# Optimization experiments

Measured on AMD Instinct MI355X. Metric: run time of the kernel, lower is better.

The kernel has to match this reference:

```python
import jax, jax.numpy as jnp
import numpy as np

K = 3  # spatial window (window_size = [1,3,3,1])


def _extract_patches(x, k):
    """TF-style extract_patches, VALID padding, stride 1, rate 1.
    x: [B,H,W,C] -> [B,Ho,Wo,k*k*C] with depth ordering (ki, kj, c)."""
    B, H, W, C = x.shape
    Ho, Wo = H - k + 1, W - k + 1
    cols = [x[:, ki:ki + Ho, kj:kj + Wo, :] for ki in range(k) for kj in range(k)]
    return jnp.concatenate(cols, axis=-1)


def setup_inputs() -> dict:
    key = jax.random.key(0)
    k1, k2 = jax.random.split(key)
    x = jax.random.normal(k1, (8, 32, 32, 32), dtype=jnp.float32)
    # weight shape per build(): (1, 1, 1, K*K*C, filters) = (1,1,1,288,64)
    w = jax.random.normal(k2, (1, 1, 1, 3 * 3 * 32, 64), dtype=jnp.float32) * 0.05
    bias = jnp.zeros((64,), dtype=jnp.float32)
    return {"x": x, "w": w, "bias": bias}


def reference(x, w, bias):
    # patches: [B,Ho,Wo,KKC]
    p = _extract_patches(x, K)
    # broadcast add: [B,Ho,Wo,KKC,1] + [KKC,F] -> [B,Ho,Wo,KKC,F]
    r = p[..., None] + w[0, 0, 0]
    # tropical conv: max-plus minus min-plus over the patch axis, plus bias
    return jnp.max(r, axis=3) - jnp.min(r, axis=3) + bias
```

## Files before the change

### kernel.cpp

```cpp
#include <hip/hip_runtime.h>
#include <math.h>


__global__ __launch_bounds__(256) void trop_kernel(
    const float* __restrict__ x, const float* __restrict__ w,
    const float* __restrict__ bias, float* __restrict__ out) {
  __shared__ float wl[96 * 64];

  const int jg = blockIdx.x;
  const int i = blockIdx.y;
  const int b = blockIdx.z;
  const int tid = threadIdx.x;
  const int f = tid & 63;
  const int jwu = __builtin_amdgcn_readfirstlane(tid >> 6) * 4;
  const int j0 = jg * 14 + jwu;

  float mx[4] = {-INFINITY, -INFINITY, -INFINITY, -INFINITY};
  float mn[4] = {INFINITY, INFINITY, INFINITY, INFINITY};

  for (int ki = 0; ki < 3; ++ki) {
    __syncthreads();
    const float4* wg = (const float4*)(w + ki * 96 * 64);
    float4* wld = (float4*)wl;
#pragma unroll
    for (int t = 0; t < 6; ++t) wld[tid + t * 256] = wg[tid + t * 256];
    __syncthreads();

    const float* xr = x + (((size_t)b * 32 + (i + ki)) * 32 + j0) * 32;

#pragma unroll
    for (int c8 = 0; c8 < 32; c8 += 8) {
      float4 xa[6][2];
#pragma unroll
      for (int col = 0; col < 6; ++col) {
        xa[col][0] = *(const float4*)(xr + col * 32 + c8);
        xa[col][1] = *(const float4*)(xr + col * 32 + c8 + 4);
      }
      const float* wbase = &wl[c8 * 64 + f];
#pragma unroll
      for (int c = 0; c < 8; ++c) {
        float w0 = wbase[c * 64];
        float w1 = wbase[32 * 64 + c * 64];
        float w2 = wbase[64 * 64 + c * 64];
        float xv[6];
#pragma unroll
        for (int col = 0; col < 6; ++col)
          xv[col] = ((const float*)xa[col])[c];
#pragma unroll
        for (int p = 0; p < 4; ++p) {
          float a0 = xv[p + 0] + w0;
          float a1 = xv[p + 1] + w1;
          float a2 = xv[p + 2] + w2;
          mx[p] = fmaxf(mx[p], fmaxf(a0, fmaxf(a1, a2)));
          mn[p] = fminf(mn[p], fminf(a0, fminf(a1, a2)));
        }
      }
    }
  }

  float bv = bias[f];
  float* ob = out + (((size_t)b * 30 + i) * 30 + j0) * 64 + f;
#pragma unroll
  for (int p = 0; p < 4; ++p) ob[p * 64] = mx[p] - mn[p] + bv;
}

extern "C" void kernel_launch(void* const* d_in, const int* in_sizes, int n_in,
                              void* d_out, int out_size, void* d_ws, size_t ws_size,
                              hipStream_t stream) {
  const float* x = (const float*)d_in[0];
  const float* w = (const float*)d_in[1];
  const float* bias = (const float*)d_in[2];
  float* out = (float*)d_out;
  dim3 grid(2, 30, 8);
  dim3 block(256);
  hipLaunchKernelGGL(trop_kernel, grid, block, 0, stream, x, w, bias, out);
}
```

Baseline: 69.60 us.

## Transpose weights in LDS per filter and cover full row per 512-thread block

Stores the weight slice in LDS transposed per filter with a padded stride so each thread reads its weights as float4 vectors instead of scalar strided loads. Each block now has 8 waves covering a whole output row (32 columns, with clamping and masked stores for the 30 valid ones), halving the grid and the number of times weights are staged into LDS. The transposed layout costs uncoalesced scalar global weight loads during staging and some wasted work on the padded columns.

```diff
diff --git a/kernel.cpp b/kernel.cpp
--- a/kernel.cpp
+++ b/kernel.cpp
@@ -2,55 +2,69 @@
 #include <math.h>
 
 
-__global__ __launch_bounds__(256) void trop_kernel(
+#define WSTRIDE 100
+
+__global__ __launch_bounds__(512) void trop_kernel(
     const float* __restrict__ x, const float* __restrict__ w,
     const float* __restrict__ bias, float* __restrict__ out) {
-  __shared__ float wl[96 * 64];
+  __shared__ float wt[64 * WSTRIDE];
 
-  const int jg = blockIdx.x;
-  const int i = blockIdx.y;
-  const int b = blockIdx.z;
+  const int i = blockIdx.x;
+  const int b = blockIdx.y;
   const int tid = threadIdx.x;
   const int f = tid & 63;
-  const int jwu = __builtin_amdgcn_readfirstlane(tid >> 6) * 4;
-  const int j0 = jg * 14 + jwu;
+  const int j0 = __builtin_amdgcn_readfirstlane(tid >> 6) * 4;
+
+  const int skq = tid >> 6;
 
   float mx[4] = {-INFINITY, -INFINITY, -INFINITY, -INFINITY};
   float mn[4] = {INFINITY, INFINITY, INFINITY, INFINITY};
+  float bv = bias[f];
 
   for (int ki = 0; ki < 3; ++ki) {
     __syncthreads();
-    const float4* wg = (const float4*)(w + ki * 96 * 64);
-    float4* wld = (float4*)wl;
 #pragma unroll
-    for (int t = 0; t < 6; ++t) wld[tid + t * 256] = wg[tid + t * 256];
+    for (int it = 0; it < 3; ++it) {
+      int k0 = (it * 8 + skq) * 4;
+      float4 v;
+      v.x = w[(ki * 96 + k0 + 0) * 64 + f];
+      v.y = w[(ki * 96 + k0 + 1) * 64 + f];
+      v.z = w[(ki * 96 + k0 + 2) * 64 + f];
+      v.w = w[(ki * 96 + k0 + 3) * 64 + f];
+      *(float4*)(&wt[f * WSTRIDE + k0]) = v;
+    }
     __syncthreads();
 
-    const float* xr = x + (((size_t)b * 32 + (i + ki)) * 32 + j0) * 32;
+    const float* xr = x + (((size_t)b * 32 + (i + ki)) * 32) * 32;
+    int cc[6];
+#pragma unroll
+    for (int col = 0; col < 6; ++col) cc[col] = (j0 + col < 32) ? j0 + col : 31;
 
 #pragma unroll
     for (int c8 = 0; c8 < 32; c8 += 8) {
       float4 xa[6][2];
 #pragma unroll
       for (int col = 0; col < 6; ++col) {
-        xa[col][0] = *(const float4*)(xr + col * 32 + c8);
-        xa[col][1] = *(const float4*)(xr + col * 32 + c8 + 4);
+        xa[col][0] = *(const float4*)(xr + cc[col] * 32 + c8);
+        xa[col][1] = *(const float4*)(xr + cc[col] * 32 + c8 + 4);
       }
-      const float* wbase = &wl[c8 * 64 + f];
+      float4 wv[3][2];
+#pragma unroll
+      for (int kj = 0; kj < 3; ++kj) {
+        const float* wrow = &wt[f * WSTRIDE + kj * 32 + c8];
+        wv[kj][0] = *(const float4*)(wrow);
+        wv[kj][1] = *(const float4*)(wrow + 4);
+      }
 #pragma unroll
       for (int c = 0; c < 8; ++c) {
-        float w0 = wbase[c * 64];
-        float w1 = wbase[32 * 64 + c * 64];
-        float w2 = wbase[64 * 64 + c * 64];
-        float xv[6];
-#pragma unroll
-        for (int col = 0; col < 6; ++col)
-          xv[col] = ((const float*)xa[col])[c];
+        float w0 = ((const float*)&wv[0][0])[c];
+        float w1 = ((const float*)&wv[1][0])[c];
+        float w2 = ((const float*)&wv[2][0])[c];
 #pragma unroll
         for (int p = 0; p < 4; ++p) {
-          float a0 = xv[p + 0] + w0;
-          float a1 = xv[p + 1] + w1;
-          float a2 = xv[p + 2] + w2;
+          float a0 = ((const float*)&xa[p + 0][0])[c] + w0;
+          float a1 = ((const float*)&xa[p + 1][0])[c] + w1;
+          float a2 = ((const float*)&xa[p + 2][0])[c] + w2;
           mx[p] = fmaxf(mx[p], fmaxf(a0, fmaxf(a1, a2)));
           mn[p] = fminf(mn[p], fminf(a0, fminf(a1, a2)));
         }
@@ -58,10 +72,10 @@
     }
   }
 
-  float bv = bias[f];
   float* ob = out + (((size_t)b * 30 + i) * 30 + j0) * 64 + f;
 #pragma unroll
-  for (int p = 0; p < 4; ++p) ob[p * 64] = mx[p] - mn[p] + bv;
+  for (int p = 0; p < 4; ++p)
+    if (j0 + p < 30) ob[(size_t)p * 64] = mx[p] - mn[p] + bv;
 }
 
 extern "C" void kernel_launch(void* const* d_in, const int* in_sizes, int n_in,
@@ -71,7 +85,7 @@
   const float* w = (const float*)d_in[1];
   const float* bias = (const float*)d_in[2];
   float* out = (float*)d_out;
-  dim3 grid(2, 30, 8);
-  dim3 block(256);
+  dim3 grid(30, 8);
+  dim3 block(512);
   hipLaunchKernelGGL(trop_kernel, grid, block, 0, stream, x, w, bias, out);
 }
```

New measurement: 68.43 us. No clear change (-1.7%).
